# Optimization experiments

Measured on AMD Instinct MI355X. Metric: run time of the kernel, lower is better.

The kernel has to match this reference:

```python
import jax, jax.numpy as jnp
import numpy as np

T, H, E, I = 1024, 2048, 64, 1024          # tokens, hidden, routed experts, expert ffn dim
N_GROUP, TOPK_GROUP, TOP_K = 8, 4, 8
N_SHARED = 2
ROUTED_SCALE = 2.5
IS = I * N_SHARED                            # shared-expert intermediate size


def setup_inputs() -> dict:
    key = jax.random.key(0)
    ks = jax.random.split(key, 8)
    s = 0.02
    return {
        "hidden_states": jax.random.normal(ks[0], (T, H), jnp.float32),
        "gate_w": jax.random.normal(ks[1], (E, H), jnp.float32) * s,
        "e_bias": jax.random.normal(ks[2], (E,), jnp.float32) * s,
        "w_gate": jax.random.normal(ks[3], (E, I, H), jnp.float32) * s,
        "w_up": jax.random.normal(ks[4], (E, I, H), jnp.float32) * s,
        "w_down": jax.random.normal(ks[5], (E, H, I), jnp.float32) * s,
        "shared_w_gate_up": jax.random.normal(ks[6], (2 * IS, H), jnp.float32) * s,
        "shared_w_down": jax.random.normal(ks[7], (H, IS), jnp.float32) * s,
    }


def _grouped_topk(scores, bias):
    """DeepSeek noaux_tc grouped top-k: sigmoid scores + correction bias,
    pick top `TOPK_GROUP` groups by sum of their top-2 biased scores,
    then top-K experts among allowed groups; weights from unbiased scores."""
    Tn, En = scores.shape
    s = scores + bias[None, :]                                   # [T, E]
    g = s.reshape(Tn, N_GROUP, En // N_GROUP)                    # [T, G, E/G]
    group_scores = jnp.sum(jax.lax.top_k(g, 2)[0], axis=-1)      # [T, G]
    _, gidx = jax.lax.top_k(group_scores, TOPK_GROUP)            # [T, topk_group]
    gmask = jnp.zeros((Tn, N_GROUP), scores.dtype).at[
        jnp.arange(Tn)[:, None], gidx].set(1.0)                  # [T, G]
    smask = jnp.repeat(gmask, En // N_GROUP, axis=1)             # [T, E]
    masked = jnp.where(smask > 0, s, -jnp.inf)
    _, topk_ids = jax.lax.top_k(masked, TOP_K)                   # [T, K]
    w = jnp.take_along_axis(scores, topk_ids, axis=1)            # unbiased scores
    w = w / jnp.sum(w, axis=-1, keepdims=True)                   # renormalize (norm_topk_prob)
    return w, topk_ids


def reference(hidden_states, gate_w, e_bias, w_gate, w_up, w_down,
              shared_w_gate_up, shared_w_down):
    x = hidden_states                                            # [T, H]
    router_logits = x @ gate_w.T                                 # [T, E]
    scores = jax.nn.sigmoid(router_logits)
    topk_w, topk_ids = _grouped_topk(scores, e_bias)             # [T, K] each
    # sparse combine weights [T, E] (zero for unselected experts)
    cw = jnp.zeros((x.shape[0], E), x.dtype).at[
        jnp.arange(x.shape[0])[:, None], topk_ids].add(topk_w)
    # routed experts: dense grouped-GEMM form of the fused-MoE math
    g = jnp.einsum('th,eih->tei', x, w_gate)                     # [T, E, I]
    u = jnp.einsum('th,eih->tei', x, w_up)
    h = jax.nn.silu(g) * u
    routed = jnp.einsum('tei,te,ehi->th', h, cw, w_down)         # [T, H]
    # shared experts MLP (SiluAndMul)
    sg_u = x @ shared_w_gate_up.T                                # [T, 2*IS]
    sg, su = jnp.split(sg_u, 2, axis=-1)
    shared = (jax.nn.silu(sg) * su) @ shared_w_down.T            # [T, H]
    return routed * ROUTED_SCALE + shared
```

## Files before the change

kernel.cpp:

```cpp
#include <hip/hip_runtime.h>
#include <hip/hip_bf16.h>
#include <math.h>

#define T_TOK 1024
#define HID   2048
#define NEXP  64
#define IDIM  1024
#define ISH   2048
#define TOPK  8

typedef float  f32x4  __attribute__((ext_vector_type(4)));
typedef __bf16 bf16x8 __attribute__((ext_vector_type(8)));

#define BM  128
#define BN_ 64
#define BK  64

#define BARRIER_NODRAIN() asm volatile("s_waitcnt lgkmcnt(0)\n\ts_barrier" ::: "memory")

__device__ __forceinline__ bf16x8 cvt8(f32x4 a, f32x4 b) {
  bf16x8 v;
  v[0]=(__bf16)a[0]; v[1]=(__bf16)a[1]; v[2]=(__bf16)a[2]; v[3]=(__bf16)a[3];
  v[4]=(__bf16)b[0]; v[5]=(__bf16)b[1]; v[6]=(__bf16)b[2]; v[7]=(__bf16)b[3];
  return v;
}

__global__ void init_kernel(int* counts) {
  if (threadIdx.x < NEXP) counts[threadIdx.x] = 0;
}

__global__ void xcast_kernel(const float* __restrict__ x, __bf16* __restrict__ xb) {
  long i = ((long)blockIdx.x * 256 + threadIdx.x) * 8;
  f32x4 a = *(const f32x4*)(x + i);
  f32x4 b = *(const f32x4*)(x + i + 4);
  *(bf16x8*)(xb + i) = cvt8(a, b);
}

__global__ __launch_bounds__(256)
void router_kernel(const float* __restrict__ x, const float* __restrict__ gw,
                   const float* __restrict__ eb,
                   int* __restrict__ ids, float* __restrict__ wts,
                   int* __restrict__ counts)
{
  __shared__ __align__(16) float xs[HID];
  __shared__ float red[256];
  __shared__ float sc[NEXP], sb[NEXP];
  const int t = blockIdx.x, tid = threadIdx.x;

  const f32x4* xsrc = (const f32x4*)(x + (long)t * HID);
  f32x4* xd = (f32x4*)xs;
  xd[tid]       = xsrc[tid];
  xd[tid + 256] = xsrc[tid + 256];
  __syncthreads();

  const int e = tid & 63, part = tid >> 6;
  const f32x4* wrow = (const f32x4*)(gw + (long)e * HID + part * 512);
  const f32x4* xrow = (const f32x4*)(xs + part * 512);
  float s = 0.f;
  #pragma unroll 4
  for (int j = 0; j < 128; ++j) {
    f32x4 wv = wrow[j], xv = xrow[j];
    s += wv[0]*xv[0] + wv[1]*xv[1] + wv[2]*xv[2] + wv[3]*xv[3];
  }
  red[tid] = s;
  __syncthreads();
  if (part == 0) {
    float logit = red[e] + red[e+64] + red[e+128] + red[e+192];
    float sig = 1.f / (1.f + expf(-logit));
    sc[e] = sig; sb[e] = sig + eb[e];
  }
  __syncthreads();

  if (tid == 0) {
    float gsc[8];
    for (int g = 0; g < 8; ++g) {
      float m1 = -1e30f, m2 = -1e30f;
      for (int j = 0; j < 8; ++j) {
        float v = sb[g*8 + j];
        if (v > m1) { m2 = m1; m1 = v; } else if (v > m2) m2 = v;
      }
      gsc[g] = m1 + m2;
    }
    unsigned gmask = 0;
    for (int it = 0; it < 4; ++it) {
      int best = 0; float bv = -1e30f;
      for (int g = 0; g < 8; ++g)
        if (!((gmask >> g) & 1) && gsc[g] > bv) { bv = gsc[g]; best = g; }
      gmask |= 1u << best;
    }
    unsigned long long taken = 0;
    int id8[8]; float wsum = 0.f;
    for (int it = 0; it < 8; ++it) {
      int best = 0; float bv = -1e30f;
      for (int e2 = 0; e2 < 64; ++e2) {
        if (!((gmask >> (e2 >> 3)) & 1)) continue;
        if ((taken >> e2) & 1) continue;
        float v = sb[e2];
        if (v > bv) { bv = v; best = e2; }
      }
      taken |= 1ull << best;
      id8[it] = best; wsum += sc[best];
    }
    float inv = 2.5f / wsum;
    for (int k = 0; k < 8; ++k) {
      ids[t*8 + k] = id8[k];
      wts[t*8 + k] = sc[id8[k]] * inv;
      atomicAdd(&counts[id8[k]], 1);
    }
  }
}

__global__ void scan_kernel(const int* __restrict__ counts,
                            int* __restrict__ seg_off, int* __restrict__ cursors,
                            int* __restrict__ pair_e, int* __restrict__ pair_mt,
                            int* __restrict__ npairs) {
  if (threadIdx.x == 0) {
    int off = 0, np = 0;
    for (int e = 0; e < NEXP; ++e) {
      seg_off[e] = off; cursors[e] = off;
      int c = counts[e]; off += c;
      for (int m = 0; m * BM < c; ++m) { pair_e[np] = e; pair_mt[np] = m; ++np; }
    }
    npairs[0] = np;
  }
}

__global__ void scatter_kernel(const int* __restrict__ ids, const float* __restrict__ wts,
                               int* __restrict__ cursors,
                               int* __restrict__ tok_list, float* __restrict__ wgt_list) {
  int idx = blockIdx.x * 256 + threadIdx.x;
  if (idx >= T_TOK * TOPK) return;
  int t = idx >> 3;
  int e = ids[idx];
  int pos = atomicAdd(&cursors[e], 1);
  tok_list[pos] = t;
  wgt_list[pos] = wts[idx];
}

template<int EPI, bool ROUTED>
__global__ __launch_bounds__(256, 3)
void gemm_stream(const __bf16* __restrict__ A, const float* __restrict__ B0,
                 long strideBe, int ldB, int K,
                 void* __restrict__ Cout, int ldc,
                 const int* __restrict__ pair_e, const int* __restrict__ pair_mt,
                 const int* __restrict__ npairs,
                 const int* __restrict__ seg_off, const int* __restrict__ seg_cnt,
                 const int* __restrict__ tok_list,
                 int Mfull)
{
  const int tid  = threadIdx.x;
  const int lane = tid & 63;
  const int wv   = tid >> 6;

  int e, mt0, soff, cnt;
  if (ROUTED) {
    int p = blockIdx.y;
    if (p >= npairs[0]) return;
    e = pair_e[p]; mt0 = pair_mt[p]; soff = seg_off[e]; cnt = seg_cnt[e];
  } else {
    e = 0; mt0 = blockIdx.y; soff = 0; cnt = Mfull;
  }
  const int rem = cnt - mt0 * BM;
  if (rem <= 0) return;

  const float* Bp = B0 + (long)e * strideBe
                  + (long)(blockIdx.x * BN_ + wv * 16 + (lane & 15)) * ldB
                  + ((lane >> 4) * 8);

  __shared__ __align__(16) __bf16 Abuf[2][BM * BK];

  const __bf16* aptr[4];
  int aoff[4];
  #pragma unroll
  for (int i = 0; i < 4; ++i) {
    int c = tid + i * 256, r = c >> 3, s = c & 7;
    int rr = (r < rem) ? r : (rem - 1);
    int base = soff + mt0 * BM + rr;
    int arow = (EPI == 0 && ROUTED) ? tok_list[base] : base;
    aptr[i] = A + (long)arow * K + s * 8;
    aoff[i] = r * 64 + ((s ^ (r & 7)) * 8);
  }

  f32x4 acc[8] = {};
  bf16x8 aR[4];
  f32x4 bA[4], bB[4];

#define LOAD_A(k) { _Pragma("unroll") \
  for (int i = 0; i < 4; ++i) aR[i] = *(const bf16x8*)(aptr[i] + (k)); }
#define STORE_A(b) { _Pragma("unroll") \
  for (int i = 0; i < 4; ++i) *(bf16x8*)&Abuf[b][aoff[i]] = aR[i]; }
#define LOAD_B(dst, k) { \
  dst[0] = *(const f32x4*)(Bp + (k));      dst[1] = *(const f32x4*)(Bp + (k) + 4); \
  dst[2] = *(const f32x4*)(Bp + (k) + 32); dst[3] = *(const f32x4*)(Bp + (k) + 36); }
#define COMPUTE(bsrc, b) { _Pragma("unroll") \
  for (int ch = 0; ch < 2; ++ch) { \
    bf16x8 bfrag = cvt8(bsrc[ch*2], bsrc[ch*2+1]); \
    const int ro = ((lane & 15) * 64) + ((((ch*4) + (lane >> 4)) ^ (lane & 7)) * 8); \
    _Pragma("unroll") \
    for (int m = 0; m < 8; ++m) { \
      bf16x8 af = *(const bf16x8*)&Abuf[b][m * 1024 + ro]; \
      acc[m] = __builtin_amdgcn_mfma_f32_16x16x32_bf16(af, bfrag, acc[m], 0, 0, 0); \
    } \
  } }

  LOAD_A(0);
  LOAD_B(bA, 0);
  const int NT = K / BK;
  for (int t = 0; t < NT; t += 2) {
    const int k1 = (t + 1 < NT) ? (t + 1) * BK : 0;
    const int k2 = (t + 2 < NT) ? (t + 2) * BK : 0;
    STORE_A(0);
    LOAD_A(k1); LOAD_B(bB, k1);
    BARRIER_NODRAIN();
    COMPUTE(bA, 0);
    STORE_A(1);
    LOAD_A(k2); LOAD_B(bA, k2);
    BARRIER_NODRAIN();
    COMPUTE(bB, 1);
  }
#undef LOAD_A
#undef STORE_A
#undef LOAD_B
#undef COMPUTE

  if (EPI == 0) {
    __syncthreads();
    __bf16* Cs = &Abuf[0][0];
    #pragma unroll
    for (int m = 0; m < 8; ++m) {
      #pragma unroll
      for (int r = 0; r < 4; ++r) {
        int row = m * 16 + (lane >> 4) * 4 + r;
        Cs[row * 64 + wv * 16 + (lane & 15)] = (__bf16)acc[m][r];
      }
    }
    __syncthreads();
    __bf16* Cb = (__bf16*)Cout;
    #pragma unroll
    for (int p = 0; p < 4; ++p) {
      int row = p * 32 + (tid >> 3);
      if (row < rem)
        *(bf16x8*)(Cb + (long)(soff + mt0 * BM + row) * ldc + blockIdx.x * BN_ + (tid & 7) * 8) =
            *(const bf16x8*)&Cs[row * 64 + (tid & 7) * 8];
    }
  } else {
    float* Of = (float*)Cout;
    const int col = blockIdx.x * BN_ + wv * 16 + (lane & 15);
    #pragma unroll
    for (int m = 0; m < 8; ++m) {
      #pragma unroll
      for (int r = 0; r < 4; ++r) {
        int row = m * 16 + (lane >> 4) * 4 + r;
        if (row < rem) {
          if (EPI == 1) {
            int orow = tok_list[soff + mt0 * BM + row];
            atomicAdd(Of + (long)orow * HID + col, acc[m][r]);
          } else {
            Of[(long)(mt0 * BM + row) * HID + col] = acc[m][r];
          }
        }
      }
    }
  }
}

__global__ void fuse_kernel(__bf16* __restrict__ g, const __bf16* __restrict__ u,
                            const float* __restrict__ wrow, int rshift) {
  long idx = ((long)blockIdx.x * 256 + threadIdx.x) * 8;
  bf16x8 gv = *(bf16x8*)(g + idx);
  bf16x8 uv = *(const bf16x8*)(u + idx);
  float w = wrow ? wrow[idx >> rshift] : 1.f;
  bf16x8 h;
  #pragma unroll
  for (int j = 0; j < 8; ++j) {
    float gf = (float)gv[j], uf = (float)uv[j];
    h[j] = (__bf16)(w * gf * uf / (1.f + __expf(-gf)));
  }
  *(bf16x8*)(g + idx) = h;
}

extern "C" void kernel_launch(void* const* d_in, const int* in_sizes, int n_in,
                              void* d_out, int out_size, void* d_ws, size_t ws_size,
                              hipStream_t stream) {
  const float* x      = (const float*)d_in[0];
  const float* gate_w = (const float*)d_in[1];
  const float* e_bias = (const float*)d_in[2];
  const float* w_gate = (const float*)d_in[3];
  const float* w_up   = (const float*)d_in[4];
  const float* w_down = (const float*)d_in[5];
  const float* sw_gu  = (const float*)d_in[6];
  const float* sw_d   = (const float*)d_in[7];
  float* out = (float*)d_out;
  char* ws = (char*)d_ws;

  size_t off = 0;
  __bf16* x_bf = (__bf16*)(ws + off);        off += (size_t)T_TOK * HID * 2;
  int*    ids  = (int*)(ws + off);           off += T_TOK * TOPK * 4;
  float*  wts  = (float*)(ws + off);         off += T_TOK * TOPK * 4;
  int* counts  = (int*)(ws + off);           off += 256;
  int* segoff  = (int*)(ws + off);           off += 256;
  int* cursors = (int*)(ws + off);           off += 256;
  int* pair_e  = (int*)(ws + off);           off += 1024;
  int* pair_mt = (int*)(ws + off);           off += 1024;
  int* npairs  = (int*)(ws + off);           off += 256;
  int* tok_list = (int*)(ws + off);          off += T_TOK * TOPK * 4;
  float* wgt_list = (float*)(ws + off);      off += T_TOK * TOPK * 4;
  off = (off + 255) & ~(size_t)255;
  __bf16* g_buf = (__bf16*)(ws + off);       off += (size_t)T_TOK * TOPK * IDIM * 2;
  __bf16* u_buf = (__bf16*)(ws + off);       off += (size_t)T_TOK * TOPK * IDIM * 2;
  __bf16* gs_buf = (__bf16*)(ws + off);      off += (size_t)T_TOK * ISH * 2;
  __bf16* us_buf = (__bf16*)(ws + off);      off += (size_t)T_TOK * ISH * 2;

  init_kernel<<<1, 64, 0, stream>>>(counts);
  xcast_kernel<<<(T_TOK * HID) / (256 * 8), 256, 0, stream>>>(x, x_bf);
  router_kernel<<<T_TOK, 256, 0, stream>>>(x, gate_w, e_bias, ids, wts, counts);
  scan_kernel<<<1, 64, 0, stream>>>(counts, segoff, cursors, pair_e, pair_mt, npairs);
  scatter_kernel<<<(T_TOK * TOPK + 255) / 256, 256, 0, stream>>>(ids, wts, cursors, tok_list, wgt_list);

  gemm_stream<0, true><<<dim3(IDIM / BN_, 128), 256, 0, stream>>>(
      x_bf, w_gate, (long)IDIM * HID, HID, HID, g_buf, IDIM,
      pair_e, pair_mt, npairs, segoff, counts, tok_list, 0);
  gemm_stream<0, true><<<dim3(IDIM / BN_, 128), 256, 0, stream>>>(
      x_bf, w_up, (long)IDIM * HID, HID, HID, u_buf, IDIM,
      pair_e, pair_mt, npairs, segoff, counts, tok_list, 0);
  fuse_kernel<<<(T_TOK * TOPK * IDIM) / (256 * 8), 256, 0, stream>>>(g_buf, u_buf, wgt_list, 10);

  gemm_stream<0, false><<<dim3(ISH / BN_, T_TOK / BM), 256, 0, stream>>>(
      x_bf, sw_gu, 0, HID, HID, gs_buf, ISH,
      nullptr, nullptr, nullptr, nullptr, nullptr, nullptr, T_TOK);
  gemm_stream<0, false><<<dim3(ISH / BN_, T_TOK / BM), 256, 0, stream>>>(
      x_bf, sw_gu + (size_t)ISH * HID, 0, HID, HID, us_buf, ISH,
      nullptr, nullptr, nullptr, nullptr, nullptr, nullptr, T_TOK);
  fuse_kernel<<<(T_TOK * ISH) / (256 * 8), 256, 0, stream>>>(gs_buf, us_buf, nullptr, 11);

  gemm_stream<2, false><<<dim3(HID / BN_, T_TOK / BM), 256, 0, stream>>>(
      gs_buf, sw_d, 0, ISH, ISH, out, HID,
      nullptr, nullptr, nullptr, nullptr, nullptr, nullptr, T_TOK);

  gemm_stream<1, true><<<dim3(HID / BN_, 128), 256, 0, stream>>>(
      g_buf, w_down, (long)HID * IDIM, IDIM, IDIM, out, HID,
      pair_e, pair_mt, npairs, segoff, counts, tok_list, 0);
}
```

Before: 722.2 us.

## Fuse gate/up GEMMs with SiLU epilogue and replace atomic down-proj with combine

Gate and up projections are computed in one kernel that shares the A tile and applies the weighted SiLU-and-mul in the epilogue, which removes the separate fuse kernels and the g/u intermediate buffers. The routed down projection now writes bf16 per-slot outputs, and a combine kernel sums the top-k rows per token through a new pos_of map, replacing float atomics. The M tile shrinks from 128 to 64 and the down kernel's occupancy hint rises to 4. In exchange, fp32 B weights are reloaded twice as often, the bf16 y buffer adds memory traffic, and rounding y to bf16 before summation adds error.

```diff
diff --git a/kernel.cpp b/kernel.cpp
--- a/kernel.cpp
+++ b/kernel.cpp
@@ -12,7 +12,7 @@
 typedef float  f32x4  __attribute__((ext_vector_type(4)));
 typedef __bf16 bf16x8 __attribute__((ext_vector_type(8)));
 
-#define BM  128
+#define BM  64
 #define BN_ 64
 #define BK  64
 
@@ -127,7 +127,8 @@
 
 __global__ void scatter_kernel(const int* __restrict__ ids, const float* __restrict__ wts,
                                int* __restrict__ cursors,
-                               int* __restrict__ tok_list, float* __restrict__ wgt_list) {
+                               int* __restrict__ tok_list, float* __restrict__ wgt_list,
+                               int* __restrict__ pos_of) {
   int idx = blockIdx.x * 256 + threadIdx.x;
   if (idx >= T_TOK * TOPK) return;
   int t = idx >> 3;
@@ -135,18 +136,19 @@
   int pos = atomicAdd(&cursors[e], 1);
   tok_list[pos] = t;
   wgt_list[pos] = wts[idx];
-}
-
-template<int EPI, bool ROUTED>
+  pos_of[idx] = pos;
+}
+
+template<bool ROUTED>
 __global__ __launch_bounds__(256, 3)
-void gemm_stream(const __bf16* __restrict__ A, const float* __restrict__ B0,
-                 long strideBe, int ldB, int K,
-                 void* __restrict__ Cout, int ldc,
-                 const int* __restrict__ pair_e, const int* __restrict__ pair_mt,
-                 const int* __restrict__ npairs,
-                 const int* __restrict__ seg_off, const int* __restrict__ seg_cnt,
-                 const int* __restrict__ tok_list,
-                 int Mfull)
+void gu_kernel(const __bf16* __restrict__ A, const float* __restrict__ Bg0,
+               const float* __restrict__ Bu0, long strideBe, int ldB, int K,
+               __bf16* __restrict__ Hout, int ldh,
+               const int* __restrict__ pair_e, const int* __restrict__ pair_mt,
+               const int* __restrict__ npairs,
+               const int* __restrict__ seg_off, const int* __restrict__ seg_cnt,
+               const int* __restrict__ tok_list, const float* __restrict__ wgt_list,
+               int Mfull)
 {
   const int tid  = threadIdx.x;
   const int lane = tid & 63;
@@ -163,41 +165,155 @@
   const int rem = cnt - mt0 * BM;
   if (rem <= 0) return;
 
-  const float* Bp = B0 + (long)e * strideBe
-                  + (long)(blockIdx.x * BN_ + wv * 16 + (lane & 15)) * ldB
-                  + ((lane >> 4) * 8);
+  const long bcol = (long)(blockIdx.x * BN_ + wv * 16 + (lane & 15));
+  const float* Bg = Bg0 + (long)e * strideBe + bcol * ldB + ((lane >> 4) * 8);
+  const float* Bu = Bu0 + (long)e * strideBe + bcol * ldB + ((lane >> 4) * 8);
 
   __shared__ __align__(16) __bf16 Abuf[2][BM * BK];
-
-  const __bf16* aptr[4];
-  int aoff[4];
+  __shared__ float Ws[BM];
+
+  const __bf16* aptr[2];
+  int aoff[2];
   #pragma unroll
-  for (int i = 0; i < 4; ++i) {
+  for (int i = 0; i < 2; ++i) {
     int c = tid + i * 256, r = c >> 3, s = c & 7;
     int rr = (r < rem) ? r : (rem - 1);
     int base = soff + mt0 * BM + rr;
-    int arow = (EPI == 0 && ROUTED) ? tok_list[base] : base;
+    int arow = ROUTED ? tok_list[base] : base;
     aptr[i] = A + (long)arow * K + s * 8;
     aoff[i] = r * 64 + ((s ^ (r & 7)) * 8);
   }
 
-  f32x4 acc[8] = {};
-  bf16x8 aR[4];
+  f32x4 ag[4] = {}, au[4] = {};
+  bf16x8 aR[2];
+  f32x4 gA[4], gB[4], uA[4], uB[4];
+
+#define LOAD_A(k) { _Pragma("unroll") \
+  for (int i = 0; i < 2; ++i) aR[i] = *(const bf16x8*)(aptr[i] + (k)); }
+#define STORE_A(b) { _Pragma("unroll") \
+  for (int i = 0; i < 2; ++i) *(bf16x8*)&Abuf[b][aoff[i]] = aR[i]; }
+#define LOAD_BP(ptr, dst, k) { \
+  dst[0] = *(const f32x4*)(ptr + (k));      dst[1] = *(const f32x4*)(ptr + (k) + 4); \
+  dst[2] = *(const f32x4*)(ptr + (k) + 32); dst[3] = *(const f32x4*)(ptr + (k) + 36); }
+#define COMPUTE(gs, us, b) { _Pragma("unroll") \
+  for (int ch = 0; ch < 2; ++ch) { \
+    bf16x8 bg = cvt8(gs[ch*2], gs[ch*2+1]); \
+    bf16x8 bu = cvt8(us[ch*2], us[ch*2+1]); \
+    const int ro = ((lane & 15) * 64) + ((((ch*4) + (lane >> 4)) ^ (lane & 7)) * 8); \
+    _Pragma("unroll") \
+    for (int m = 0; m < 4; ++m) { \
+      bf16x8 af = *(const bf16x8*)&Abuf[b][m * 1024 + ro]; \
+      ag[m] = __builtin_amdgcn_mfma_f32_16x16x32_bf16(af, bg, ag[m], 0, 0, 0); \
+      au[m] = __builtin_amdgcn_mfma_f32_16x16x32_bf16(af, bu, au[m], 0, 0, 0); \
+    } \
+  } }
+
+  LOAD_A(0);
+  LOAD_BP(Bg, gA, 0); LOAD_BP(Bu, uA, 0);
+  const int NT = K / BK;
+  for (int t = 0; t < NT; t += 2) {
+    const int k1 = (t + 1 < NT) ? (t + 1) * BK : 0;
+    const int k2 = (t + 2 < NT) ? (t + 2) * BK : 0;
+    STORE_A(0);
+    LOAD_A(k1); LOAD_BP(Bg, gB, k1); LOAD_BP(Bu, uB, k1);
+    BARRIER_NODRAIN();
+    COMPUTE(gA, uA, 0);
+    STORE_A(1);
+    LOAD_A(k2); LOAD_BP(Bg, gA, k2); LOAD_BP(Bu, uA, k2);
+    BARRIER_NODRAIN();
+    COMPUTE(gB, uB, 1);
+  }
+#undef LOAD_A
+#undef STORE_A
+#undef LOAD_BP
+#undef COMPUTE
+
+  if (tid < BM) {
+    int rr = (tid < rem) ? tid : (rem - 1);
+    Ws[tid] = ROUTED ? wgt_list[soff + mt0 * BM + rr] : 1.f;
+  }
+  __syncthreads();
+  __bf16* Cs = &Abuf[0][0];
+  #pragma unroll
+  for (int m = 0; m < 4; ++m) {
+    #pragma unroll
+    for (int r = 0; r < 4; ++r) {
+      int row = m * 16 + (lane >> 4) * 4 + r;
+      float g = ag[m][r], u = au[m][r];
+      float h = Ws[row] * g * u / (1.f + __expf(-g));
+      Cs[row * 64 + wv * 16 + (lane & 15)] = (__bf16)h;
+    }
+  }
+  __syncthreads();
+  {
+    int row = tid >> 2;
+    if (row < rem) {
+      __bf16* dst = Hout + (long)(soff + mt0 * BM + row) * ldh + blockIdx.x * BN_;
+      #pragma unroll
+      for (int j = 0; j < 2; ++j) {
+        int c8 = (tid & 3) * 2 + j;
+        *(bf16x8*)(dst + c8 * 8) = *(const bf16x8*)&Cs[row * 64 + c8 * 8];
+      }
+    }
+  }
+}
+
+template<int EPI>
+__global__ __launch_bounds__(256, 4)
+void down_kernel(const __bf16* __restrict__ A, const float* __restrict__ B0,
+                 long strideBe, int ldB, int K, void* __restrict__ Out, int ldc,
+                 const int* __restrict__ pair_e, const int* __restrict__ pair_mt,
+                 const int* __restrict__ npairs,
+                 const int* __restrict__ seg_off, const int* __restrict__ seg_cnt,
+                 int Mfull)
+{
+  const int tid  = threadIdx.x;
+  const int lane = tid & 63;
+  const int wv   = tid >> 6;
+
+  int e, mt0, soff, cnt;
+  if (EPI == 1) {
+    int p = blockIdx.y;
+    if (p >= npairs[0]) return;
+    e = pair_e[p]; mt0 = pair_mt[p]; soff = seg_off[e]; cnt = seg_cnt[e];
+  } else {
+    e = 0; mt0 = blockIdx.y; soff = 0; cnt = Mfull;
+  }
+  const int rem = cnt - mt0 * BM;
+  if (rem <= 0) return;
+
+  const long bcol = (long)(blockIdx.x * BN_ + wv * 16 + (lane & 15));
+  const float* Bp = B0 + (long)e * strideBe + bcol * ldB + ((lane >> 4) * 8);
+
+  __shared__ __align__(16) __bf16 Abuf[2][BM * BK];
+
+  const __bf16* aptr[2];
+  int aoff[2];
+  #pragma unroll
+  for (int i = 0; i < 2; ++i) {
+    int c = tid + i * 256, r = c >> 3, s = c & 7;
+    int rr = (r < rem) ? r : (rem - 1);
+    aptr[i] = A + (long)(soff + mt0 * BM + rr) * K + s * 8;
+    aoff[i] = r * 64 + ((s ^ (r & 7)) * 8);
+  }
+
+  f32x4 acc[4] = {};
+  bf16x8 aR[2];
   f32x4 bA[4], bB[4];
 
 #define LOAD_A(k) { _Pragma("unroll") \
-  for (int i = 0; i < 4; ++i) aR[i] = *(const bf16x8*)(aptr[i] + (k)); }
+  for (int i = 0; i < 2; ++i) aR[i] = *(const bf16x8*)(aptr[i] + (k)); }
 #define STORE_A(b) { _Pragma("unroll") \
-  for (int i = 0; i < 4; ++i) *(bf16x8*)&Abuf[b][aoff[i]] = aR[i]; }
+  for (int i = 0; i < 2; ++i) *(bf16x8*)&Abuf[b][aoff[i]] = aR[i]; }
 #define LOAD_B(dst, k) { \
   dst[0] = *(const f32x4*)(Bp + (k));      dst[1] = *(const f32x4*)(Bp + (k) + 4); \
   dst[2] = *(const f32x4*)(Bp + (k) + 32); dst[3] = *(const f32x4*)(Bp + (k) + 36); }
-#define COMPUTE(bsrc, b) { _Pragma("unroll") \
+#define COMPUTE(bs, b) { _Pragma("unroll") \
   for (int ch = 0; ch < 2; ++ch) { \
-    bf16x8 bfrag = cvt8(bsrc[ch*2], bsrc[ch*2+1]); \
+    bf16x8 bfrag = cvt8(bs[ch*2], bs[ch*2+1]); \
     const int ro = ((lane & 15) * 64) + ((((ch*4) + (lane >> 4)) ^ (lane & 7)) * 8); \
     _Pragma("unroll") \
-    for (int m = 0; m < 8; ++m) { \
+    for (int m = 0; m < 4; ++m) { \
       bf16x8 af = *(const bf16x8*)&Abuf[b][m * 1024 + ro]; \
       acc[m] = __builtin_amdgcn_mfma_f32_16x16x32_bf16(af, bfrag, acc[m], 0, 0, 0); \
     } \
@@ -223,11 +339,11 @@
 #undef LOAD_B
 #undef COMPUTE
 
-  if (EPI == 0) {
+  if (EPI == 1) {
     __syncthreads();
     __bf16* Cs = &Abuf[0][0];
     #pragma unroll
-    for (int m = 0; m < 8; ++m) {
+    for (int m = 0; m < 4; ++m) {
       #pragma unroll
       for (int r = 0; r < 4; ++r) {
         int row = m * 16 + (lane >> 4) * 4 + r;
@@ -235,48 +351,47 @@
       }
     }
     __syncthreads();
-    __bf16* Cb = (__bf16*)Cout;
-    #pragma unroll
-    for (int p = 0; p < 4; ++p) {
-      int row = p * 32 + (tid >> 3);
-      if (row < rem)
-        *(bf16x8*)(Cb + (long)(soff + mt0 * BM + row) * ldc + blockIdx.x * BN_ + (tid & 7) * 8) =
-            *(const bf16x8*)&Cs[row * 64 + (tid & 7) * 8];
+    int row = tid >> 2;
+    if (row < rem) {
+      __bf16* dst = (__bf16*)Out + (long)(soff + mt0 * BM + row) * ldc + blockIdx.x * BN_;
+      #pragma unroll
+      for (int j = 0; j < 2; ++j) {
+        int c8 = (tid & 3) * 2 + j;
+        *(bf16x8*)(dst + c8 * 8) = *(const bf16x8*)&Cs[row * 64 + c8 * 8];
+      }
     }
   } else {
-    float* Of = (float*)Cout;
+    float* O = (float*)Out;
     const int col = blockIdx.x * BN_ + wv * 16 + (lane & 15);
     #pragma unroll
-    for (int m = 0; m < 8; ++m) {
+    for (int m = 0; m < 4; ++m) {
       #pragma unroll
       for (int r = 0; r < 4; ++r) {
         int row = m * 16 + (lane >> 4) * 4 + r;
-        if (row < rem) {
-          if (EPI == 1) {
-            int orow = tok_list[soff + mt0 * BM + row];
-            atomicAdd(Of + (long)orow * HID + col, acc[m][r]);
-          } else {
-            Of[(long)(mt0 * BM + row) * HID + col] = acc[m][r];
-          }
-        }
-      }
-    }
-  }
-}
-
-__global__ void fuse_kernel(__bf16* __restrict__ g, const __bf16* __restrict__ u,
-                            const float* __restrict__ wrow, int rshift) {
-  long idx = ((long)blockIdx.x * 256 + threadIdx.x) * 8;
-  bf16x8 gv = *(bf16x8*)(g + idx);
-  bf16x8 uv = *(const bf16x8*)(u + idx);
-  float w = wrow ? wrow[idx >> rshift] : 1.f;
-  bf16x8 h;
+        if (row < rem)
+          O[(long)(mt0 * BM + row) * ldc + col] = acc[m][r];
+      }
+    }
+  }
+}
+
+__global__ __launch_bounds__(256)
+void combine_kernel(const __bf16* __restrict__ y, const int* __restrict__ pos_of,
+                    float* __restrict__ out) {
+  const int t = blockIdx.x;
+  const int c0 = threadIdx.x * 8;
+  float* orow = out + (long)t * HID + c0;
+  f32x4 s0 = *(const f32x4*)orow;
+  f32x4 s1 = *(const f32x4*)(orow + 4);
   #pragma unroll
-  for (int j = 0; j < 8; ++j) {
-    float gf = (float)gv[j], uf = (float)uv[j];
-    h[j] = (__bf16)(w * gf * uf / (1.f + __expf(-gf)));
-  }
-  *(bf16x8*)(g + idx) = h;
+  for (int k = 0; k < TOPK; ++k) {
+    int row = pos_of[t * TOPK + k];
+    bf16x8 v = *(const bf16x8*)(y + (long)row * HID + c0);
+    s0[0] += (float)v[0]; s0[1] += (float)v[1]; s0[2] += (float)v[2]; s0[3] += (float)v[3];
+    s1[0] += (float)v[4]; s1[1] += (float)v[5]; s1[2] += (float)v[6]; s1[3] += (float)v[7];
+  }
+  *(f32x4*)orow = s0;
+  *(f32x4*)(orow + 4) = s1;
 }
 
 extern "C" void kernel_launch(void* const* d_in, const int* in_sizes, int n_in,
@@ -305,39 +420,34 @@
   int* npairs  = (int*)(ws + off);           off += 256;
   int* tok_list = (int*)(ws + off);          off += T_TOK * TOPK * 4;
   float* wgt_list = (float*)(ws + off);      off += T_TOK * TOPK * 4;
+  int* pos_of  = (int*)(ws + off);           off += T_TOK * TOPK * 4;
   off = (off + 255) & ~(size_t)255;
-  __bf16* g_buf = (__bf16*)(ws + off);       off += (size_t)T_TOK * TOPK * IDIM * 2;
-  __bf16* u_buf = (__bf16*)(ws + off);       off += (size_t)T_TOK * TOPK * IDIM * 2;
-  __bf16* gs_buf = (__bf16*)(ws + off);      off += (size_t)T_TOK * ISH * 2;
-  __bf16* us_buf = (__bf16*)(ws + off);      off += (size_t)T_TOK * ISH * 2;
+  __bf16* h_buf  = (__bf16*)(ws + off);      off += (size_t)T_TOK * TOPK * IDIM * 2;
+  __bf16* hs_buf = (__bf16*)(ws + off);      off += (size_t)T_TOK * ISH * 2;
+  __bf16* y_buf  = (__bf16*)(ws + off);      off += (size_t)T_TOK * TOPK * HID * 2;
 
   init_kernel<<<1, 64, 0, stream>>>(counts);
   xcast_kernel<<<(T_TOK * HID) / (256 * 8), 256, 0, stream>>>(x, x_bf);
   router_kernel<<<T_TOK, 256, 0, stream>>>(x, gate_w, e_bias, ids, wts, counts);
   scan_kernel<<<1, 64, 0, stream>>>(counts, segoff, cursors, pair_e, pair_mt, npairs);
-  scatter_kernel<<<(T_TOK * TOPK + 255) / 256, 256, 0, stream>>>(ids, wts, cursors, tok_list, wgt_list);
-
-  gemm_stream<0, true><<<dim3(IDIM / BN_, 128), 256, 0, stream>>>(
-      x_bf, w_gate, (long)IDIM * HID, HID, HID, g_buf, IDIM,
-      pair_e, pair_mt, npairs, segoff, counts, tok_list, 0);
-  gemm_stream<0, true><<<dim3(IDIM / BN_, 128), 256, 0, stream>>>(
-      x_bf, w_up, (long)IDIM * HID, HID, HID, u_buf, IDIM,
-      pair_e, pair_mt, npairs, segoff, counts, tok_list, 0);
-  fuse_kernel<<<(T_TOK * TOPK * IDIM) / (256 * 8), 256, 0, stream>>>(g_buf, u_buf, wgt_list, 10);
-
-  gemm_stream<0, false><<<dim3(ISH / BN_, T_TOK / BM), 256, 0, stream>>>(
-      x_bf, sw_gu, 0, HID, HID, gs_buf, ISH,
-      nullptr, nullptr, nullptr, nullptr, nullptr, nullptr, T_TOK);
-  gemm_stream<0, false><<<dim3(ISH / BN_, T_TOK / BM), 256, 0, stream>>>(
-      x_bf, sw_gu + (size_t)ISH * HID, 0, HID, HID, us_buf, ISH,
-      nullptr, nullptr, nullptr, nullptr, nullptr, nullptr, T_TOK);
-  fuse_kernel<<<(T_TOK * ISH) / (256 * 8), 256, 0, stream>>>(gs_buf, us_buf, nullptr, 11);
-
-  gemm_stream<2, false><<<dim3(HID / BN_, T_TOK / BM), 256, 0, stream>>>(
-      gs_buf, sw_d, 0, ISH, ISH, out, HID,
-      nullptr, nullptr, nullptr, nullptr, nullptr, nullptr, T_TOK);
-
-  gemm_stream<1, true><<<dim3(HID / BN_, 128), 256, 0, stream>>>(
-      g_buf, w_down, (long)HID * IDIM, IDIM, IDIM, out, HID,
-      pair_e, pair_mt, npairs, segoff, counts, tok_list, 0);
-}
+  scatter_kernel<<<(T_TOK * TOPK + 255) / 256, 256, 0, stream>>>(
+      ids, wts, cursors, tok_list, wgt_list, pos_of);
+
+  gu_kernel<true><<<dim3(IDIM / BN_, 256), 256, 0, stream>>>(
+      x_bf, w_gate, w_up, (long)IDIM * HID, HID, HID, h_buf, IDIM,
+      pair_e, pair_mt, npairs, segoff, counts, tok_list, wgt_list, 0);
+
+  gu_kernel<false><<<dim3(ISH / BN_, T_TOK / BM), 256, 0, stream>>>(
+      x_bf, sw_gu, sw_gu + (size_t)ISH * HID, 0, HID, HID, hs_buf, ISH,
+      nullptr, nullptr, nullptr, nullptr, nullptr, nullptr, nullptr, T_TOK);
+
+  down_kernel<2><<<dim3(HID / BN_, T_TOK / BM), 256, 0, stream>>>(
+      hs_buf, sw_d, 0, ISH, ISH, out, HID,
+      nullptr, nullptr, nullptr, nullptr, nullptr, T_TOK);
+
+  down_kernel<1><<<dim3(HID / BN_, 256), 256, 0, stream>>>(
+      h_buf, w_down, (long)HID * IDIM, IDIM, IDIM, y_buf, HID,
+      pair_e, pair_mt, npairs, segoff, counts, 0);
+
+  combine_kernel<<<T_TOK, 256, 0, stream>>>(y_buf, pos_of, out);
+}
```

New measurement: 783.6 us. 8.5% more time.

## Use direct global-to-LDS triple-buffered GEMM, merge gate/up launches, replace atomics with combine

Applied to the files above, without the earlier changes.

Replaces the register-staged double-buffered GEMM with a triple-buffered pipeline that loads A and fp32 B tiles straight into LDS through global_load_lds. Gate and up projections are merged into one launch via a z-dimension of two. The routed down projection now writes per-slot bf16 outputs to a buffer instead of using fp32 atomics, and a separate combine kernel sums the top-k rows into the output. The aim is to cut register pressure and load latency and to remove atomic contention. The cost is 96KB of LDS per block, which limits occupancy to one block, plus an extra buffer and kernel, and bf16 rounding of the routed partial results.

```diff
diff --git a/kernel.cpp b/kernel.cpp
--- a/kernel.cpp
+++ b/kernel.cpp
@@ -127,7 +127,8 @@
 
 __global__ void scatter_kernel(const int* __restrict__ ids, const float* __restrict__ wts,
                                int* __restrict__ cursors,
-                               int* __restrict__ tok_list, float* __restrict__ wgt_list) {
+                               int* __restrict__ tok_list, float* __restrict__ wgt_list,
+                               int* __restrict__ pos_of) {
   int idx = blockIdx.x * 256 + threadIdx.x;
   if (idx >= T_TOK * TOPK) return;
   int t = idx >> 3;
@@ -135,22 +136,21 @@
   int pos = atomicAdd(&cursors[e], 1);
   tok_list[pos] = t;
   wgt_list[pos] = wts[idx];
-}
-
-template<int EPI, bool ROUTED>
-__global__ __launch_bounds__(256, 3)
-void gemm_stream(const __bf16* __restrict__ A, const float* __restrict__ B0,
-                 long strideBe, int ldB, int K,
-                 void* __restrict__ Cout, int ldc,
-                 const int* __restrict__ pair_e, const int* __restrict__ pair_mt,
-                 const int* __restrict__ npairs,
-                 const int* __restrict__ seg_off, const int* __restrict__ seg_cnt,
-                 const int* __restrict__ tok_list,
-                 int Mfull)
+  pos_of[idx] = pos;
+}
+
+template<int EPI, bool ROUTED, bool GATHER>
+__global__ __launch_bounds__(256, 1)
+void gemm_dma(const __bf16* __restrict__ A, const float* __restrict__ Bg0,
+              const float* __restrict__ Bu0, long strideBe, int ldB, int K,
+              void* Cg, void* Cu, int ldc,
+              const int* __restrict__ pair_e, const int* __restrict__ pair_mt,
+              const int* __restrict__ npairs,
+              const int* __restrict__ seg_off, const int* __restrict__ seg_cnt,
+              const int* __restrict__ tok_list, int Mfull)
 {
-  const int tid  = threadIdx.x;
-  const int lane = tid & 63;
-  const int wv   = tid >> 6;
+  __shared__ __align__(16) char smem[3 * 32768];
+  const int tid = threadIdx.x, lane = tid & 63, wv = tid >> 6;
 
   int e, mt0, soff, cnt;
   if (ROUTED) {
@@ -163,78 +163,86 @@
   const int rem = cnt - mt0 * BM;
   if (rem <= 0) return;
 
-  const float* Bp = B0 + (long)e * strideBe
-                  + (long)(blockIdx.x * BN_ + wv * 16 + (lane & 15)) * ldB
-                  + ((lane >> 4) * 8);
-
-  __shared__ __align__(16) __bf16 Abuf[2][BM * BK];
-
-  const __bf16* aptr[4];
-  int aoff[4];
+  const float* B0 = (gridDim.z == 2 && blockIdx.z) ? Bu0 : Bg0;
+  void* Cout      = (gridDim.z == 2 && blockIdx.z) ? Cu  : Cg;
+  const float* Bb0 = B0 + (long)e * strideBe;
+
+  const __bf16* srcA[4];
+  const float*  srcB[4];
   #pragma unroll
   for (int i = 0; i < 4; ++i) {
-    int c = tid + i * 256, r = c >> 3, s = c & 7;
-    int rr = (r < rem) ? r : (rem - 1);
-    int base = soff + mt0 * BM + rr;
-    int arow = (EPI == 0 && ROUTED) ? tok_list[base] : base;
-    aptr[i] = A + (long)arow * K + s * 8;
-    aoff[i] = r * 64 + ((s ^ (r & 7)) * 8);
-  }
+    int row = wv * 32 + i * 8 + (lane >> 3);
+    int kcA = (lane & 7) ^ (row & 7);
+    int rr  = (row < rem) ? row : (rem - 1);
+    int idx = soff + mt0 * BM + rr;
+    long arow = GATHER ? (long)tok_list[idx] : (long)idx;
+    srcA[i] = A + arow * (long)K + kcA * 8;
+
+    int col = wv * 16 + i * 4 + (lane >> 4);
+    int kcB = (lane & 15) ^ (col & 15);
+    srcB[i] = Bb0 + (long)(blockIdx.x * BN_ + col) * ldB + kcB * 4;
+  }
+
+#define STAGE(b, kk) { \
+  char* Ad = smem + (b) * 32768 + wv * 4096; \
+  char* Bd = Ad + 16384; \
+  _Pragma("unroll") \
+  for (int i = 0; i < 4; ++i) \
+    __builtin_amdgcn_global_load_lds((const __attribute__((address_space(1))) void*)(srcA[i] + (kk)), \
+        (__attribute__((address_space(3))) void*)(Ad + i * 1024), 16, 0, 0); \
+  _Pragma("unroll") \
+  for (int i = 0; i < 4; ++i) \
+    __builtin_amdgcn_global_load_lds((const __attribute__((address_space(1))) void*)(srcB[i] + (kk)), \
+        (__attribute__((address_space(3))) void*)(Bd + i * 1024), 16, 0, 0); }
 
   f32x4 acc[8] = {};
-  bf16x8 aR[4];
-  f32x4 bA[4], bB[4];
-
-#define LOAD_A(k) { _Pragma("unroll") \
-  for (int i = 0; i < 4; ++i) aR[i] = *(const bf16x8*)(aptr[i] + (k)); }
-#define STORE_A(b) { _Pragma("unroll") \
-  for (int i = 0; i < 4; ++i) *(bf16x8*)&Abuf[b][aoff[i]] = aR[i]; }
-#define LOAD_B(dst, k) { \
-  dst[0] = *(const f32x4*)(Bp + (k));      dst[1] = *(const f32x4*)(Bp + (k) + 4); \
-  dst[2] = *(const f32x4*)(Bp + (k) + 32); dst[3] = *(const f32x4*)(Bp + (k) + 36); }
-#define COMPUTE(bsrc, b) { _Pragma("unroll") \
-  for (int ch = 0; ch < 2; ++ch) { \
-    bf16x8 bfrag = cvt8(bsrc[ch*2], bsrc[ch*2+1]); \
-    const int ro = ((lane & 15) * 64) + ((((ch*4) + (lane >> 4)) ^ (lane & 7)) * 8); \
+  const int c15 = lane & 15, hi = lane >> 4;
+
+#define COMPUTE(b) { \
+  char* Ab = smem + (b) * 32768; \
+  char* Bbuf = Ab + 16384; \
+  _Pragma("unroll") \
+  for (int kh = 0; kh < 2; ++kh) { \
+    const int colL = wv * 16 + c15; \
+    const int kc = kh * 8 + hi * 2; \
+    f32x4 b0 = *(const f32x4*)(Bbuf + colL * 256 + (((kc    ) ^ c15) << 4)); \
+    f32x4 b1 = *(const f32x4*)(Bbuf + colL * 256 + (((kc + 1) ^ c15) << 4)); \
+    bf16x8 bfrag = cvt8(b0, b1); \
+    const int physA = ((kh * 4 + hi) ^ (lane & 7)) << 4; \
     _Pragma("unroll") \
     for (int m = 0; m < 8; ++m) { \
-      bf16x8 af = *(const bf16x8*)&Abuf[b][m * 1024 + ro]; \
+      bf16x8 af = *(const bf16x8*)(Ab + (m * 16 + c15) * 128 + physA); \
       acc[m] = __builtin_amdgcn_mfma_f32_16x16x32_bf16(af, bfrag, acc[m], 0, 0, 0); \
     } \
   } }
 
-  LOAD_A(0);
-  LOAD_B(bA, 0);
   const int NT = K / BK;
-  for (int t = 0; t < NT; t += 2) {
-    const int k1 = (t + 1 < NT) ? (t + 1) * BK : 0;
-    const int k2 = (t + 2 < NT) ? (t + 2) * BK : 0;
-    STORE_A(0);
-    LOAD_A(k1); LOAD_B(bB, k1);
+  STAGE(0, 0);
+  STAGE(1, BK);
+  for (int t = 0; t < NT; ++t) {
+    asm volatile("s_waitcnt vmcnt(8)" ::: "memory");
     BARRIER_NODRAIN();
-    COMPUTE(bA, 0);
-    STORE_A(1);
-    LOAD_A(k2); LOAD_B(bA, k2);
-    BARRIER_NODRAIN();
-    COMPUTE(bB, 1);
-  }
-#undef LOAD_A
-#undef STORE_A
-#undef LOAD_B
+    const int kk = (t + 2 < NT) ? (t + 2) * BK : 0;
+    STAGE((t + 2) % 3, kk);
+    COMPUTE(t % 3);
+  }
+#undef STAGE
 #undef COMPUTE
 
+  asm volatile("s_waitcnt vmcnt(0)" ::: "memory");
+  BARRIER_NODRAIN();
+
   if (EPI == 0) {
-    __syncthreads();
-    __bf16* Cs = &Abuf[0][0];
+    __bf16* Cs = (__bf16*)smem;
     #pragma unroll
     for (int m = 0; m < 8; ++m) {
       #pragma unroll
       for (int r = 0; r < 4; ++r) {
-        int row = m * 16 + (lane >> 4) * 4 + r;
-        Cs[row * 64 + wv * 16 + (lane & 15)] = (__bf16)acc[m][r];
+        int row = m * 16 + hi * 4 + r;
+        Cs[row * 64 + wv * 16 + c15] = (__bf16)acc[m][r];
       }
     }
-    __syncthreads();
+    BARRIER_NODRAIN();
     __bf16* Cb = (__bf16*)Cout;
     #pragma unroll
     for (int p = 0; p < 4; ++p) {
@@ -244,21 +252,15 @@
             *(const bf16x8*)&Cs[row * 64 + (tid & 7) * 8];
     }
   } else {
-    float* Of = (float*)Cout;
-    const int col = blockIdx.x * BN_ + wv * 16 + (lane & 15);
+    float* O = (float*)Cout;
+    const int col = blockIdx.x * BN_ + wv * 16 + c15;
     #pragma unroll
     for (int m = 0; m < 8; ++m) {
       #pragma unroll
       for (int r = 0; r < 4; ++r) {
-        int row = m * 16 + (lane >> 4) * 4 + r;
-        if (row < rem) {
-          if (EPI == 1) {
-            int orow = tok_list[soff + mt0 * BM + row];
-            atomicAdd(Of + (long)orow * HID + col, acc[m][r]);
-          } else {
-            Of[(long)(mt0 * BM + row) * HID + col] = acc[m][r];
-          }
-        }
+        int row = m * 16 + hi * 4 + r;
+        if (row < rem)
+          O[(long)(mt0 * BM + row) * ldc + col] = acc[m][r];
       }
     }
   }
@@ -277,6 +279,25 @@
     h[j] = (__bf16)(w * gf * uf / (1.f + __expf(-gf)));
   }
   *(bf16x8*)(g + idx) = h;
+}
+
+__global__ __launch_bounds__(256)
+void combine_kernel(const __bf16* __restrict__ y, const int* __restrict__ pos_of,
+                    float* __restrict__ out) {
+  const int t = blockIdx.x;
+  const int c0 = threadIdx.x * 8;
+  float* orow = out + (long)t * HID + c0;
+  f32x4 s0 = *(const f32x4*)orow;
+  f32x4 s1 = *(const f32x4*)(orow + 4);
+  #pragma unroll
+  for (int k = 0; k < TOPK; ++k) {
+    int row = pos_of[t * TOPK + k];
+    bf16x8 v = *(const bf16x8*)(y + (long)row * HID + c0);
+    s0[0] += (float)v[0]; s0[1] += (float)v[1]; s0[2] += (float)v[2]; s0[3] += (float)v[3];
+    s1[0] += (float)v[4]; s1[1] += (float)v[5]; s1[2] += (float)v[6]; s1[3] += (float)v[7];
+  }
+  *(f32x4*)orow = s0;
+  *(f32x4*)(orow + 4) = s1;
 }
 
 extern "C" void kernel_launch(void* const* d_in, const int* in_sizes, int n_in,
@@ -305,39 +326,39 @@
   int* npairs  = (int*)(ws + off);           off += 256;
   int* tok_list = (int*)(ws + off);          off += T_TOK * TOPK * 4;
   float* wgt_list = (float*)(ws + off);      off += T_TOK * TOPK * 4;
+  int* pos_of  = (int*)(ws + off);           off += T_TOK * TOPK * 4;
   off = (off + 255) & ~(size_t)255;
-  __bf16* g_buf = (__bf16*)(ws + off);       off += (size_t)T_TOK * TOPK * IDIM * 2;
-  __bf16* u_buf = (__bf16*)(ws + off);       off += (size_t)T_TOK * TOPK * IDIM * 2;
+  __bf16* g_buf  = (__bf16*)(ws + off);      off += (size_t)T_TOK * TOPK * IDIM * 2;
+  __bf16* u_buf  = (__bf16*)(ws + off);      off += (size_t)T_TOK * TOPK * IDIM * 2;
   __bf16* gs_buf = (__bf16*)(ws + off);      off += (size_t)T_TOK * ISH * 2;
   __bf16* us_buf = (__bf16*)(ws + off);      off += (size_t)T_TOK * ISH * 2;
+  __bf16* y_buf  = (__bf16*)(ws + off);      off += (size_t)T_TOK * TOPK * HID * 2;
 
   init_kernel<<<1, 64, 0, stream>>>(counts);
   xcast_kernel<<<(T_TOK * HID) / (256 * 8), 256, 0, stream>>>(x, x_bf);
   router_kernel<<<T_TOK, 256, 0, stream>>>(x, gate_w, e_bias, ids, wts, counts);
   scan_kernel<<<1, 64, 0, stream>>>(counts, segoff, cursors, pair_e, pair_mt, npairs);
-  scatter_kernel<<<(T_TOK * TOPK + 255) / 256, 256, 0, stream>>>(ids, wts, cursors, tok_list, wgt_list);
-
-  gemm_stream<0, true><<<dim3(IDIM / BN_, 128), 256, 0, stream>>>(
-      x_bf, w_gate, (long)IDIM * HID, HID, HID, g_buf, IDIM,
+  scatter_kernel<<<(T_TOK * TOPK + 255) / 256, 256, 0, stream>>>(
+      ids, wts, cursors, tok_list, wgt_list, pos_of);
+
+  gemm_dma<0, true, true><<<dim3(IDIM / BN_, 128, 2), 256, 0, stream>>>(
+      x_bf, w_gate, w_up, (long)IDIM * HID, HID, HID, g_buf, u_buf, IDIM,
       pair_e, pair_mt, npairs, segoff, counts, tok_list, 0);
-  gemm_stream<0, true><<<dim3(IDIM / BN_, 128), 256, 0, stream>>>(
-      x_bf, w_up, (long)IDIM * HID, HID, HID, u_buf, IDIM,
-      pair_e, pair_mt, npairs, segoff, counts, tok_list, 0);
+
   fuse_kernel<<<(T_TOK * TOPK * IDIM) / (256 * 8), 256, 0, stream>>>(g_buf, u_buf, wgt_list, 10);
 
-  gemm_stream<0, false><<<dim3(ISH / BN_, T_TOK / BM), 256, 0, stream>>>(
-      x_bf, sw_gu, 0, HID, HID, gs_buf, ISH,
-      nullptr, nullptr, nullptr, nullptr, nullptr, nullptr, T_TOK);
-  gemm_stream<0, false><<<dim3(ISH / BN_, T_TOK / BM), 256, 0, stream>>>(
-      x_bf, sw_gu + (size_t)ISH * HID, 0, HID, HID, us_buf, ISH,
+  gemm_dma<0, false, false><<<dim3(ISH / BN_, T_TOK / BM, 2), 256, 0, stream>>>(
+      x_bf, sw_gu, sw_gu + (size_t)ISH * HID, 0, HID, HID, gs_buf, us_buf, ISH,
       nullptr, nullptr, nullptr, nullptr, nullptr, nullptr, T_TOK);
   fuse_kernel<<<(T_TOK * ISH) / (256 * 8), 256, 0, stream>>>(gs_buf, us_buf, nullptr, 11);
 
-  gemm_stream<2, false><<<dim3(HID / BN_, T_TOK / BM), 256, 0, stream>>>(
-      gs_buf, sw_d, 0, ISH, ISH, out, HID,
+  gemm_dma<2, false, false><<<dim3(HID / BN_, T_TOK / BM, 1), 256, 0, stream>>>(
+      gs_buf, sw_d, sw_d, 0, ISH, ISH, out, out, HID,
       nullptr, nullptr, nullptr, nullptr, nullptr, nullptr, T_TOK);
 
-  gemm_stream<1, true><<<dim3(HID / BN_, 128), 256, 0, stream>>>(
-      g_buf, w_down, (long)HID * IDIM, IDIM, IDIM, out, HID,
+  gemm_dma<0, true, false><<<dim3(HID / BN_, 128, 1), 256, 0, stream>>>(
+      g_buf, w_down, w_down, (long)HID * IDIM, IDIM, IDIM, y_buf, y_buf, HID,
       pair_e, pair_mt, npairs, segoff, counts, tok_list, 0);
-}
+
+  combine_kernel<<<T_TOK, 256, 0, stream>>>(y_buf, pos_of, out);
+}
```

Measured after the change: 653.4 us. 9.5% less time.
